# Kernel tuning notes

Measured on AMD Instinct MI355X. Metric: run time of the kernel, lower is better.

Reference implementation:

```python
import jax, jax.numpy as jnp
import numpy as np

B, T = 512, 2048
IN1, H1, H2 = 1, 64, 16


def _lstm_params(key, in_dim, hid):
    k = 1.0 / np.sqrt(hid)
    ks = jax.random.split(key, 4)
    u = lambda kk, shape: jax.random.uniform(kk, shape, jnp.float32, -k, k)
    return (u(ks[0], (4 * hid, in_dim)),  # w_ih, PyTorch gate order i,f,g,o
            u(ks[1], (4 * hid, hid)),     # w_hh
            u(ks[2], (4 * hid,)),         # b_ih
            u(ks[3], (4 * hid,)))         # b_hh


def setup_inputs() -> dict:
    key = jax.random.key(0)
    kx, k1, k2 = jax.random.split(key, 3)
    x = jax.random.normal(kx, (B, T, IN1), dtype=jnp.float32)
    w_ih1, w_hh1, b_ih1, b_hh1 = _lstm_params(k1, IN1, H1)
    w_ih2, w_hh2, b_ih2, b_hh2 = _lstm_params(k2, H1, H2)
    return {"x": x,
            "w_ih1": w_ih1, "w_hh1": w_hh1, "b_ih1": b_ih1, "b_hh1": b_hh1,
            "w_ih2": w_ih2, "w_hh2": w_hh2, "b_ih2": b_ih2, "b_hh2": b_hh2}


def _lstm(x, w_ih, w_hh, b_ih, b_hh):
    # x: [B, T, in]; returns all hidden states [B, T, H]
    hid = w_hh.shape[1]
    # precompute input contribution for every timestep: [T, B, 4H]
    xg = jnp.einsum('bti,gi->tbg', x, w_ih) + b_ih + b_hh
    h0 = jnp.zeros((x.shape[0], hid), x.dtype)
    c0 = jnp.zeros((x.shape[0], hid), x.dtype)

    def step(carry, xt):
        h, c = carry
        gates = xt + h @ w_hh.T                       # [B, 4H]
        i, f, g, o = jnp.split(gates, 4, axis=-1)     # PyTorch order
        i = jax.nn.sigmoid(i)
        f = jax.nn.sigmoid(f)
        g = jnp.tanh(g)
        o = jax.nn.sigmoid(o)
        c = f * c + i * g
        h = o * jnp.tanh(c)
        return (h, c), h

    _, hs = jax.lax.scan(step, (h0, c0), xg)          # hs: [T, B, H]
    return jnp.transpose(hs, (1, 0, 2))               # [B, T, H]


def reference(x, w_ih1, w_hh1, b_ih1, b_hh1, w_ih2, w_hh2, b_ih2, b_hh2):
    h1 = _lstm(x, w_ih1, w_hh1, b_ih1, b_hh1)   # [B, T, 64]
    h2 = _lstm(h1, w_ih2, w_hh2, b_ih2, b_hh2)  # [B, T, 16]
    return h2
```

## Files before the change

kernel.cpp:

```cpp
#include <hip/hip_runtime.h>

#define TSTEPS 2048
#define NBATCH 512
#define H1 64
#define H2 16

typedef _Float16 h2v __attribute__((ext_vector_type(2)));

__device__ __forceinline__ float fsig(float x) {
    return __builtin_amdgcn_rcpf(1.0f + __builtin_amdgcn_exp2f(-1.4426950408889634f * x));
}
__device__ __forceinline__ float ftanh(float x) {
    return 1.0f - 2.0f * __builtin_amdgcn_rcpf(1.0f + __builtin_amdgcn_exp2f(2.8853900817779268f * x));
}
__device__ __forceinline__ float act(float x, float k2) {
    return k2 * fsig(k2 * x) - (k2 - 1.0f);
}

#if __has_builtin(__builtin_amdgcn_fdot2)
__device__ __forceinline__ float dot2(int wp, int hp, float acc) {
    return __builtin_amdgcn_fdot2(__builtin_bit_cast(h2v, wp),
                                  __builtin_bit_cast(h2v, hp), acc, false);
}
#else
__device__ __forceinline__ float dot2(int wp, int hp, float acc) {
    h2v a = __builtin_bit_cast(h2v, wp), b = __builtin_bit_cast(h2v, hp);
    return acc + (float)a.x * (float)b.x + (float)a.y * (float)b.y;
}
#endif

__device__ __forceinline__ int packh2(float a, float b) {
    h2v v; v.x = (_Float16)a; v.y = (_Float16)b;
    return __builtin_bit_cast(int, v);
}
template<int CTRL>
__device__ __forceinline__ float dpp_bcast(float v) {
    int r = __builtin_amdgcn_mov_dpp(__float_as_int(v), CTRL, 0xF, 0xF, true);
    return __int_as_float(r);
}

__global__ void __launch_bounds__(64, 1)
__attribute__((amdgpu_waves_per_eu(1, 1)))
lstm2_fused(const float* __restrict__ x,
            const float* __restrict__ w_ih1,
            const float* __restrict__ w_hh1,
            const float* __restrict__ b_ih1,
            const float* __restrict__ b_hh1,
            const float* __restrict__ w_ih2,
            const float* __restrict__ w_hh2,
            const float* __restrict__ b_ih2,
            const float* __restrict__ b_hh2,
            float* __restrict__ out)
{
    const int lane = threadIdx.x;
    const int b    = blockIdx.x;

    __shared__ float    x_lds[TSTEPS];
    __shared__ _Float16 h1_lds[H1];
    __shared__ _Float16 h2_lds[H2];
    __shared__ float    ring[32][H2];

    {
        const float4* xs = (const float4*)(x + (size_t)b * TSTEPS);
        float4* xd = (float4*)x_lds;
        #pragma unroll
        for (int i = 0; i < 8; ++i) xd[lane + 64 * i] = xs[lane + 64 * i];
    }
    if (lane < 32) ((int*)h1_lds)[lane] = 0;
    if (lane < 8)  ((int*)h2_lds)[lane] = 0;

    int   w1[4][32];
    float wx1[4], bs1[4];
    #pragma unroll
    for (int g = 0; g < 4; ++g) {
        const int r = g * H1 + lane;
        const float* wr = w_hh1 + (size_t)r * H1;
        #pragma unroll
        for (int k = 0; k < 32; ++k) w1[g][k] = packh2(wr[2 * k], wr[2 * k + 1]);
        wx1[g] = w_ih1[r];
        bs1[g] = b_ih1[r] + b_hh1[r];
    }
    const int m  = lane >> 2;
    const int g2 = lane & 3;
    const int r2 = g2 * H2 + m;
    int w2[32], wh2[8];
    #pragma unroll
    for (int k = 0; k < 32; ++k)
        w2[k] = packh2(w_ih2[(size_t)r2 * H1 + 2 * k], w_ih2[(size_t)r2 * H1 + 2 * k + 1]);
    #pragma unroll
    for (int k = 0; k < 8; ++k)
        wh2[k] = packh2(w_hh2[(size_t)r2 * H2 + 2 * k], w_hh2[(size_t)r2 * H2 + 2 * k + 1]);
    const float bs2 = b_ih2[r2] + b_hh2[r2];
    const float k22 = (g2 == 2) ? 2.0f : 1.0f;

    float c1 = 0.0f;
    float c2 = 0.0f;
    float* outb = out + (size_t)b * TSTEPS * H2;

    for (int p = 0; p <= TSTEPS; ++p) {
        #pragma unroll
        for (int g = 0; g < 4; ++g)
            #pragma unroll
            for (int k = 0; k < 32; ++k) asm volatile("" : "+v"(w1[g][k]));
        #pragma unroll
        for (int k = 0; k < 32; ++k) asm volatile("" : "+v"(w2[k]));
        #pragma unroll
        for (int k = 0; k < 8; ++k)  asm volatile("" : "+v"(wh2[k]));

        const int tau_f = p - 1;
        if (tau_f >= 31 && (tau_f & 15) == 15) {
            const int tau0 = (tau_f & ~15) - 16;
            const int tt = tau0 + (lane >> 2), ch0 = (lane & 3) * 4;
            float4 v = *(const float4*)&ring[tt & 31][ch0];
            *(float4*)(outb + (size_t)tt * H2 + ch0) = v;
        }

        int hp[32];
        {
            const int4* hs = (const int4*)h1_lds;
            #pragma unroll
            for (int i = 0; i < 8; ++i) {
                int4 v = hs[i];
                hp[4*i+0] = v.x; hp[4*i+1] = v.y; hp[4*i+2] = v.z; hp[4*i+3] = v.w;
            }
        }

        if (p < TSTEPS) {
            const float xv = x_lds[p];
            float ai = bs1[0] + wx1[0] * xv;
            float af = bs1[1] + wx1[1] * xv;
            float ag = bs1[2] + wx1[2] * xv;
            float ao = bs1[3] + wx1[3] * xv;
            #pragma unroll
            for (int k = 0; k < 32; ++k) {
                ai = dot2(w1[0][k], hp[k], ai);
                af = dot2(w1[1][k], hp[k], af);
                ag = dot2(w1[2][k], hp[k], ag);
                ao = dot2(w1[3][k], hp[k], ao);
            }
            float gi = fsig(ai), gf = fsig(af), gg = ftanh(ag), go = fsig(ao);
            c1 = gf * c1 + gi * gg;
            float h1n = go * ftanh(c1);
            h1_lds[lane] = (_Float16)h1n;
        }

        if (p >= 1) {
            int hq[8];
            {
                const int4* hs = (const int4*)h2_lds;
                int4 u0 = hs[0], u1 = hs[1];
                hq[0]=u0.x; hq[1]=u0.y; hq[2]=u0.z; hq[3]=u0.w;
                hq[4]=u1.x; hq[5]=u1.y; hq[6]=u1.z; hq[7]=u1.w;
            }
            float a0 = bs2, a1 = 0.f, a2a = 0.f, a3 = 0.f;
            #pragma unroll
            for (int k = 0; k < 8; ++k) {
                a0  = dot2(w2[4*k+0], hp[4*k+0], a0);
                a1  = dot2(w2[4*k+1], hp[4*k+1], a1);
                a2a = dot2(w2[4*k+2], hp[4*k+2], a2a);
                a3  = dot2(w2[4*k+3], hp[4*k+3], a3);
            }
            #pragma unroll
            for (int k = 0; k < 2; ++k) {
                a0  = dot2(wh2[4*k+0], hq[4*k+0], a0);
                a1  = dot2(wh2[4*k+1], hq[4*k+1], a1);
                a2a = dot2(wh2[4*k+2], hq[4*k+2], a2a);
                a3  = dot2(wh2[4*k+3], hq[4*k+3], a3);
            }
            float av = act((a0 + a1) + (a2a + a3), k22);
            float gi = dpp_bcast<0x00>(av);
            float gf = dpp_bcast<0x55>(av);
            float gg = dpp_bcast<0xAA>(av);
            float go = dpp_bcast<0xFF>(av);
            c2 = gf * c2 + gi * gg;
            float h2n = go * ftanh(c2);
            if (g2 == 0) {
                h2_lds[m] = (_Float16)h2n;
                ring[(p - 1) & 31][m] = h2n;
            }
        }
    }

    {
        const int tt = 2032 + (lane >> 2), ch0 = (lane & 3) * 4;
        float4 v = *(const float4*)&ring[tt & 31][ch0];
        *(float4*)(outb + (size_t)tt * H2 + ch0) = v;
    }
}

extern "C" void kernel_launch(void* const* d_in, const int* in_sizes, int n_in,
                              void* d_out, int out_size, void* d_ws, size_t ws_size,
                              hipStream_t stream) {
    const float* x     = (const float*)d_in[0];
    const float* w_ih1 = (const float*)d_in[1];
    const float* w_hh1 = (const float*)d_in[2];
    const float* b_ih1 = (const float*)d_in[3];
    const float* b_hh1 = (const float*)d_in[4];
    const float* w_ih2 = (const float*)d_in[5];
    const float* w_hh2 = (const float*)d_in[6];
    const float* b_ih2 = (const float*)d_in[7];
    const float* b_hh2 = (const float*)d_in[8];
    float* out = (float*)d_out;

    lstm2_fused<<<NBATCH, 64, 0, stream>>>(x, w_ih1, w_hh1, b_ih1, b_hh1,
                                           w_ih2, w_hh2, b_ih2, b_hh2, out);
}
```

Measured before the change: 1.234 ms.

## Interleave layer-1 and layer-2 dot products with chunked LDS loads, pin weights in AGPRs

The layer-1 and layer-2 input-projection dot products now run in one loop over chunks of h1. Each chunk's LDS load is issued one iteration ahead so load latency hides behind the dot2 math, instead of loading all of h1 into registers up front. The layer-2 weights are pinned to accumulator registers (AGPRs) via inline asm constraints, and the occupancy attribute is replaced by a 256-VGPR cap to ease register pressure. The risk is extra AGPR-to-VGPR copies each step, and the layer-1 dot product now also runs on the final extra step (p == TSTEPS) with a wrapped x index.

```diff
diff --git a/kernel.cpp b/kernel.cpp
--- a/kernel.cpp
+++ b/kernel.cpp
@@ -40,7 +40,7 @@
 }
 
 __global__ void __launch_bounds__(64, 1)
-__attribute__((amdgpu_waves_per_eu(1, 1)))
+__attribute__((amdgpu_num_vgpr(256)))
 lstm2_fused(const float* __restrict__ x,
             const float* __restrict__ w_ih1,
             const float* __restrict__ w_hh1,
@@ -103,9 +103,9 @@
             #pragma unroll
             for (int k = 0; k < 32; ++k) asm volatile("" : "+v"(w1[g][k]));
         #pragma unroll
-        for (int k = 0; k < 32; ++k) asm volatile("" : "+v"(w2[k]));
-        #pragma unroll
-        for (int k = 0; k < 8; ++k)  asm volatile("" : "+v"(wh2[k]));
+        for (int k = 0; k < 32; ++k) asm volatile("" : "+a"(w2[k]));
+        #pragma unroll
+        for (int k = 0; k < 8; ++k)  asm volatile("" : "+a"(wh2[k]));
 
         const int tau_f = p - 1;
         if (tau_f >= 31 && (tau_f & 15) == 15) {
@@ -115,29 +115,47 @@
             *(float4*)(outb + (size_t)tt * H2 + ch0) = v;
         }
 
-        int hp[32];
+        const float xv = x_lds[p & (TSTEPS - 1)];
+        float ai = bs1[0] + wx1[0] * xv;
+        float af = bs1[1] + wx1[1] * xv;
+        float ag = bs1[2] + wx1[2] * xv;
+        float ao = bs1[3] + wx1[3] * xv;
+        float a0 = bs2, a1 = 0.f, a2a = 0.f, a3 = 0.f;
+
         {
-            const int4* hs = (const int4*)h1_lds;
+            const int4* hs4 = (const int4*)h1_lds;
+            int4 hA = hs4[0], hB = hs4[1];
             #pragma unroll
-            for (int i = 0; i < 8; ++i) {
-                int4 v = hs[i];
-                hp[4*i+0] = v.x; hp[4*i+1] = v.y; hp[4*i+2] = v.z; hp[4*i+3] = v.w;
+            for (int c = 0; c < 4; ++c) {
+                int4 nA, nB;
+                if (c < 3) { nA = hs4[2 * c + 2]; nB = hs4[2 * c + 3]; }
+                const int h0 = hA.x, h1p = hA.y, h2p = hA.z, h3p = hA.w;
+                const int h4p = hB.x, h5p = hB.y, h6p = hB.z, h7p = hB.w;
+                ai = dot2(w1[0][8*c+0], h0, ai);  af = dot2(w1[1][8*c+0], h0, af);
+                ag = dot2(w1[2][8*c+0], h0, ag);  ao = dot2(w1[3][8*c+0], h0, ao);
+                ai = dot2(w1[0][8*c+1], h1p, ai); af = dot2(w1[1][8*c+1], h1p, af);
+                ag = dot2(w1[2][8*c+1], h1p, ag); ao = dot2(w1[3][8*c+1], h1p, ao);
+                ai = dot2(w1[0][8*c+2], h2p, ai); af = dot2(w1[1][8*c+2], h2p, af);
+                ag = dot2(w1[2][8*c+2], h2p, ag); ao = dot2(w1[3][8*c+2], h2p, ao);
+                ai = dot2(w1[0][8*c+3], h3p, ai); af = dot2(w1[1][8*c+3], h3p, af);
+                ag = dot2(w1[2][8*c+3], h3p, ag); ao = dot2(w1[3][8*c+3], h3p, ao);
+                ai = dot2(w1[0][8*c+4], h4p, ai); af = dot2(w1[1][8*c+4], h4p, af);
+                ag = dot2(w1[2][8*c+4], h4p, ag); ao = dot2(w1[3][8*c+4], h4p, ao);
+                ai = dot2(w1[0][8*c+5], h5p, ai); af = dot2(w1[1][8*c+5], h5p, af);
+                ag = dot2(w1[2][8*c+5], h5p, ag); ao = dot2(w1[3][8*c+5], h5p, ao);
+                ai = dot2(w1[0][8*c+6], h6p, ai); af = dot2(w1[1][8*c+6], h6p, af);
+                ag = dot2(w1[2][8*c+6], h6p, ag); ao = dot2(w1[3][8*c+6], h6p, ao);
+                ai = dot2(w1[0][8*c+7], h7p, ai); af = dot2(w1[1][8*c+7], h7p, af);
+                ag = dot2(w1[2][8*c+7], h7p, ag); ao = dot2(w1[3][8*c+7], h7p, ao);
+                a0  = dot2(w2[8*c+0], h0,  a0);   a0  = dot2(w2[8*c+4], h4p, a0);
+                a1  = dot2(w2[8*c+1], h1p, a1);   a1  = dot2(w2[8*c+5], h5p, a1);
+                a2a = dot2(w2[8*c+2], h2p, a2a);  a2a = dot2(w2[8*c+6], h6p, a2a);
+                a3  = dot2(w2[8*c+3], h3p, a3);   a3  = dot2(w2[8*c+7], h7p, a3);
+                if (c < 3) { hA = nA; hB = nB; }
             }
         }
 
         if (p < TSTEPS) {
-            const float xv = x_lds[p];
-            float ai = bs1[0] + wx1[0] * xv;
-            float af = bs1[1] + wx1[1] * xv;
-            float ag = bs1[2] + wx1[2] * xv;
-            float ao = bs1[3] + wx1[3] * xv;
-            #pragma unroll
-            for (int k = 0; k < 32; ++k) {
-                ai = dot2(w1[0][k], hp[k], ai);
-                af = dot2(w1[1][k], hp[k], af);
-                ag = dot2(w1[2][k], hp[k], ag);
-                ao = dot2(w1[3][k], hp[k], ao);
-            }
             float gi = fsig(ai), gf = fsig(af), gg = ftanh(ag), go = fsig(ao);
             c1 = gf * c1 + gi * gg;
             float h1n = go * ftanh(c1);
@@ -151,14 +169,6 @@
                 int4 u0 = hs[0], u1 = hs[1];
                 hq[0]=u0.x; hq[1]=u0.y; hq[2]=u0.z; hq[3]=u0.w;
                 hq[4]=u1.x; hq[5]=u1.y; hq[6]=u1.z; hq[7]=u1.w;
-            }
-            float a0 = bs2, a1 = 0.f, a2a = 0.f, a3 = 0.f;
-            #pragma unroll
-            for (int k = 0; k < 8; ++k) {
-                a0  = dot2(w2[4*k+0], hp[4*k+0], a0);
-                a1  = dot2(w2[4*k+1], hp[4*k+1], a1);
-                a2a = dot2(w2[4*k+2], hp[4*k+2], a2a);
-                a3  = dot2(w2[4*k+3], hp[4*k+3], a3);
             }
             #pragma unroll
             for (int k = 0; k < 2; ++k) {
```

Result: slower. 1.359 ms (+10.1%).

## Split each batch's recurrent dot products across two waves with LDS exchange

Applied to the files above, without the earlier changes.

Each block now runs two waves. Each wave holds half of the K dimension of the layer-1 and layer-2 weights and computes partial gate sums, then the waves swap partials through double-buffered LDS with a block barrier every timestep. Both waves then finish the activations redundantly and write their own copy of the hidden state. This halves the serial dot-product chain per timestep and the register pressure per lane. The cost is a __syncthreads plus LDS round trip on the critical path of every step, and 512 blocks of 128 threads instead of 64.

```diff
diff --git a/kernel.cpp b/kernel.cpp
--- a/kernel.cpp
+++ b/kernel.cpp
@@ -39,7 +39,7 @@
     return __int_as_float(r);
 }
 
-__global__ void __launch_bounds__(64, 1)
+__global__ void __launch_bounds__(128, 1)
 __attribute__((amdgpu_waves_per_eu(1, 1)))
 lstm2_fused(const float* __restrict__ x,
             const float* __restrict__ w_ih1,
@@ -52,44 +52,51 @@
             const float* __restrict__ b_hh2,
             float* __restrict__ out)
 {
-    const int lane = threadIdx.x;
+    const int tid  = threadIdx.x;
+    const int w    = tid >> 6;
+    const int lane = tid & 63;
     const int b    = blockIdx.x;
 
-    __shared__ float    x_lds[TSTEPS];
-    __shared__ _Float16 h1_lds[H1];
-    __shared__ _Float16 h2_lds[H2];
-    __shared__ float    ring[32][H2];
-
+    __shared__ __align__(16) float    x_lds[TSTEPS];
+    __shared__ __align__(16) _Float16 h1s[2][H1];
+    __shared__ __align__(16) _Float16 h2s[2][H2];
+    __shared__ __align__(16) float    xch[2][2][64][4];
+    __shared__ __align__(16) float    xch2[2][2][64];
+    __shared__ __align__(16) float    ring[32][H2];
+
+    if (tid < 64) ((int*)h1s)[tid] = 0;
+    else if (tid < 80) ((int*)h2s)[tid - 64] = 0;
     {
         const float4* xs = (const float4*)(x + (size_t)b * TSTEPS);
         float4* xd = (float4*)x_lds;
         #pragma unroll
-        for (int i = 0; i < 8; ++i) xd[lane + 64 * i] = xs[lane + 64 * i];
-    }
-    if (lane < 32) ((int*)h1_lds)[lane] = 0;
-    if (lane < 8)  ((int*)h2_lds)[lane] = 0;
-
-    int   w1[4][32];
+        for (int i = 0; i < 4; ++i) xd[tid + 128 * i] = xs[tid + 128 * i];
+    }
+    __syncthreads();
+
+    int   w1[4][16];
     float wx1[4], bs1[4];
     #pragma unroll
     for (int g = 0; g < 4; ++g) {
         const int r = g * H1 + lane;
-        const float* wr = w_hh1 + (size_t)r * H1;
+        const float* wr = w_hh1 + (size_t)r * H1 + 32 * w;
         #pragma unroll
-        for (int k = 0; k < 32; ++k) w1[g][k] = packh2(wr[2 * k], wr[2 * k + 1]);
+        for (int t = 0; t < 16; ++t) w1[g][t] = packh2(wr[2 * t], wr[2 * t + 1]);
         wx1[g] = w_ih1[r];
         bs1[g] = b_ih1[r] + b_hh1[r];
     }
     const int m  = lane >> 2;
     const int g2 = lane & 3;
     const int r2 = g2 * H2 + m;
-    int w2[32], wh2[8];
+    int w2[16], wh2[4];
     #pragma unroll
-    for (int k = 0; k < 32; ++k)
-        w2[k] = packh2(w_ih2[(size_t)r2 * H1 + 2 * k], w_ih2[(size_t)r2 * H1 + 2 * k + 1]);
+    for (int t = 0; t < 16; ++t)
+        w2[t] = packh2(w_ih2[(size_t)r2 * H1 + 32 * w + 2 * t],
+                       w_ih2[(size_t)r2 * H1 + 32 * w + 2 * t + 1]);
     #pragma unroll
-    for (int k = 0; k < 8; ++k)
-        wh2[k] = packh2(w_hh2[(size_t)r2 * H2 + 2 * k], w_hh2[(size_t)r2 * H2 + 2 * k + 1]);
+    for (int t = 0; t < 4; ++t)
+        wh2[t] = packh2(w_hh2[(size_t)r2 * H2 + 8 * w + 2 * t],
+                        w_hh2[(size_t)r2 * H2 + 8 * w + 2 * t + 1]);
     const float bs2 = b_ih2[r2] + b_hh2[r2];
     const float k22 = (g2 == 2) ? 2.0f : 1.0f;
 
@@ -97,77 +104,66 @@
     float c2 = 0.0f;
     float* outb = out + (size_t)b * TSTEPS * H2;
 
+    const int4* hs = ((const int4*)h1s[w]) + 4 * w;
+
+#define DOTP(T, HV)  do {                                   \
+        ai = dot2(w1[0][T], HV, ai);                        \
+        af = dot2(w1[1][T], HV, af);                        \
+        ag = dot2(w1[2][T], HV, ag);                        \
+        ao = dot2(w1[3][T], HV, ao);                        \
+        if ((T & 3) == 0) a0 = dot2(w2[T], HV, a0);         \
+        if ((T & 3) == 1) a1 = dot2(w2[T], HV, a1);         \
+        if ((T & 3) == 2) a2 = dot2(w2[T], HV, a2);         \
+        if ((T & 3) == 3) a3 = dot2(w2[T], HV, a3);         \
+    } while (0)
+
     for (int p = 0; p <= TSTEPS; ++p) {
-        #pragma unroll
-        for (int g = 0; g < 4; ++g)
-            #pragma unroll
-            for (int k = 0; k < 32; ++k) asm volatile("" : "+v"(w1[g][k]));
-        #pragma unroll
-        for (int k = 0; k < 32; ++k) asm volatile("" : "+v"(w2[k]));
-        #pragma unroll
-        for (int k = 0; k < 8; ++k)  asm volatile("" : "+v"(wh2[k]));
-
         const int tau_f = p - 1;
         if (tau_f >= 31 && (tau_f & 15) == 15) {
             const int tau0 = (tau_f & ~15) - 16;
-            const int tt = tau0 + (lane >> 2), ch0 = (lane & 3) * 4;
-            float4 v = *(const float4*)&ring[tt & 31][ch0];
-            *(float4*)(outb + (size_t)tt * H2 + ch0) = v;
+            const int tt = tau0 + (tid >> 3), ch0 = (tid & 7) * 2;
+            float2 v = *(const float2*)&ring[tt & 31][ch0];
+            *(float2*)(outb + (size_t)tt * H2 + ch0) = v;
         }
 
-        int hp[32];
-        {
-            const int4* hs = (const int4*)h1_lds;
-            #pragma unroll
-            for (int i = 0; i < 8; ++i) {
-                int4 v = hs[i];
-                hp[4*i+0] = v.x; hp[4*i+1] = v.y; hp[4*i+2] = v.z; hp[4*i+3] = v.w;
-            }
-        }
+        int4 hA = hs[0], hB = hs[1], hC = hs[2], hD = hs[3];
+        int4 hq = ((const int4*)h2s[w])[w];
+
+        float ai = 0.f, af = 0.f, ag = 0.f, ao = 0.f;
+        float a0 = 0.f, a1 = 0.f, a2 = 0.f, a3 = 0.f;
+        DOTP(0, hA.x);  DOTP(1, hA.y);  DOTP(2, hA.z);  DOTP(3, hA.w);
+        DOTP(4, hB.x);  DOTP(5, hB.y);  DOTP(6, hB.z);  DOTP(7, hB.w);
+        DOTP(8, hC.x);  DOTP(9, hC.y);  DOTP(10, hC.z); DOTP(11, hC.w);
+        DOTP(12, hD.x); DOTP(13, hD.y); DOTP(14, hD.z); DOTP(15, hD.w);
+        a0 = dot2(wh2[0], hq.x, a0);
+        a1 = dot2(wh2[1], hq.y, a1);
+        a2 = dot2(wh2[2], hq.z, a2);
+        a3 = dot2(wh2[3], hq.w, a3);
+        const float my2 = (a0 + a1) + (a2 + a3);
+
+        const int pb = p & 1;
+        float4 mine = {ai, af, ag, ao};
+        *(float4*)&xch[pb][w][lane][0] = mine;
+        xch2[pb][w][lane] = my2;
+        __syncthreads();
+        float4 othr = *(const float4*)&xch[pb][w ^ 1][lane][0];
+        float  o2   = xch2[pb][w ^ 1][lane];
 
         if (p < TSTEPS) {
             const float xv = x_lds[p];
-            float ai = bs1[0] + wx1[0] * xv;
-            float af = bs1[1] + wx1[1] * xv;
-            float ag = bs1[2] + wx1[2] * xv;
-            float ao = bs1[3] + wx1[3] * xv;
-            #pragma unroll
-            for (int k = 0; k < 32; ++k) {
-                ai = dot2(w1[0][k], hp[k], ai);
-                af = dot2(w1[1][k], hp[k], af);
-                ag = dot2(w1[2][k], hp[k], ag);
-                ao = dot2(w1[3][k], hp[k], ao);
-            }
-            float gi = fsig(ai), gf = fsig(af), gg = ftanh(ag), go = fsig(ao);
+            float pi = ai + othr.x + bs1[0] + wx1[0] * xv;
+            float pf = af + othr.y + bs1[1] + wx1[1] * xv;
+            float pg = ag + othr.z + bs1[2] + wx1[2] * xv;
+            float po = ao + othr.w + bs1[3] + wx1[3] * xv;
+            float gi = fsig(pi), gf = fsig(pf), gg = ftanh(pg), go = fsig(po);
             c1 = gf * c1 + gi * gg;
             float h1n = go * ftanh(c1);
-            h1_lds[lane] = (_Float16)h1n;
+            h1s[w][lane] = (_Float16)h1n;
         }
 
         if (p >= 1) {
-            int hq[8];
-            {
-                const int4* hs = (const int4*)h2_lds;
-                int4 u0 = hs[0], u1 = hs[1];
-                hq[0]=u0.x; hq[1]=u0.y; hq[2]=u0.z; hq[3]=u0.w;
-                hq[4]=u1.x; hq[5]=u1.y; hq[6]=u1.z; hq[7]=u1.w;
-            }
-            float a0 = bs2, a1 = 0.f, a2a = 0.f, a3 = 0.f;
-            #pragma unroll
-            for (int k = 0; k < 8; ++k) {
-                a0  = dot2(w2[4*k+0], hp[4*k+0], a0);
-                a1  = dot2(w2[4*k+1], hp[4*k+1], a1);
-                a2a = dot2(w2[4*k+2], hp[4*k+2], a2a);
-                a3  = dot2(w2[4*k+3], hp[4*k+3], a3);
-            }
-            #pragma unroll
-            for (int k = 0; k < 2; ++k) {
-                a0  = dot2(wh2[4*k+0], hq[4*k+0], a0);
-                a1  = dot2(wh2[4*k+1], hq[4*k+1], a1);
-                a2a = dot2(wh2[4*k+2], hq[4*k+2], a2a);
-                a3  = dot2(wh2[4*k+3], hq[4*k+3], a3);
-            }
-            float av = act((a0 + a1) + (a2a + a3), k22);
+            float pre2 = my2 + o2 + bs2;
+            float av = act(pre2, k22);
             float gi = dpp_bcast<0x00>(av);
             float gf = dpp_bcast<0x55>(av);
             float gg = dpp_bcast<0xAA>(av);
@@ -175,16 +171,19 @@
             c2 = gf * c2 + gi * gg;
             float h2n = go * ftanh(c2);
             if (g2 == 0) {
-                h2_lds[m] = (_Float16)h2n;
-                ring[(p - 1) & 31][m] = h2n;
+                h2s[w][m] = (_Float16)h2n;
+                if (w == 0) ring[(p - 1) & 31][m] = h2n;
             }
         }
     }
+#undef DOTP
+
+    __syncthreads();
 
     {
-        const int tt = 2032 + (lane >> 2), ch0 = (lane & 3) * 4;
-        float4 v = *(const float4*)&ring[tt & 31][ch0];
-        *(float4*)(outb + (size_t)tt * H2 + ch0) = v;
+        const int tt = 2032 + (tid >> 3), ch0 = (tid & 7) * 2;
+        float2 v = *(const float2*)&ring[tt & 31][ch0];
+        *(float2*)(outb + (size_t)tt * H2 + ch0) = v;
     }
 }
 
@@ -202,6 +201,6 @@
     const float* b_hh2 = (const float*)d_in[8];
     float* out = (float*)d_out;
 
-    lstm2_fused<<<NBATCH, 64, 0, stream>>>(x, w_ih1, w_hh1, b_ih1, b_hh1,
-                                           w_ih2, w_hh2, b_ih2, b_hh2, out);
-}
+    lstm2_fused<<<NBATCH, 128, 0, stream>>>(x, w_ih1, w_hh1, b_ih1, b_hh1,
+                                            w_ih2, w_hh2, b_ih2, b_hh2, out);
+}
```

Result: slower. 1.588 ms (+28.7%).

## Move g/o gate and layer-2 weights from registers into LDS

Applied to the files above, without the earlier changes.

Keeps only the input and forget gate recurrent weights in VGPRs and stages the cell and output gate weights plus layer-2 weights as packed half2 in shared memory, loading them each timestep interleaved with the dot products. It also merges the layer-2 input projection into the same loop over h1 chunks. The aim is lower register pressure and better scheduling, at the cost of extra LDS reads per step in a latency-bound recurrence.

```diff
diff --git a/kernel.cpp b/kernel.cpp
--- a/kernel.cpp
+++ b/kernel.cpp
@@ -55,6 +55,7 @@
     const int lane = threadIdx.x;
     const int b    = blockIdx.x;
 
+    __shared__ int4     wlds[26][64];
     __shared__ float    x_lds[TSTEPS];
     __shared__ _Float16 h1_lds[H1];
     __shared__ _Float16 h2_lds[H2];
@@ -69,27 +70,48 @@
     if (lane < 32) ((int*)h1_lds)[lane] = 0;
     if (lane < 8)  ((int*)h2_lds)[lane] = 0;
 
-    int   w1[4][32];
-    float wx1[4], bs1[4];
-    #pragma unroll
-    for (int g = 0; g < 4; ++g) {
-        const int r = g * H1 + lane;
-        const float* wr = w_hh1 + (size_t)r * H1;
+    int w1i[32], w1f[32];
+    {
+        const float* wri = w_hh1 + (size_t)lane * H1;
+        const float* wrf = w_hh1 + (size_t)(H1 + lane) * H1;
         #pragma unroll
-        for (int k = 0; k < 32; ++k) w1[g][k] = packh2(wr[2 * k], wr[2 * k + 1]);
-        wx1[g] = w_ih1[r];
-        bs1[g] = b_ih1[r] + b_hh1[r];
+        for (int k = 0; k < 32; ++k) {
+            w1i[k] = packh2(wri[2 * k], wri[2 * k + 1]);
+            w1f[k] = packh2(wrf[2 * k], wrf[2 * k + 1]);
+        }
     }
     const int m  = lane >> 2;
     const int g2 = lane & 3;
     const int r2 = g2 * H2 + m;
-    int w2[32], wh2[8];
-    #pragma unroll
-    for (int k = 0; k < 32; ++k)
-        w2[k] = packh2(w_ih2[(size_t)r2 * H1 + 2 * k], w_ih2[(size_t)r2 * H1 + 2 * k + 1]);
-    #pragma unroll
-    for (int k = 0; k < 8; ++k)
-        wh2[k] = packh2(w_hh2[(size_t)r2 * H2 + 2 * k], w_hh2[(size_t)r2 * H2 + 2 * k + 1]);
+    {
+        const float* wrg = w_hh1 + (size_t)(2 * H1 + lane) * H1;
+        const float* wro = w_hh1 + (size_t)(3 * H1 + lane) * H1;
+        const float* wr2 = w_ih2 + (size_t)r2 * H1;
+        #pragma unroll
+        for (int tq = 0; tq < 8; ++tq) {
+            wlds[tq][lane] = make_int4(
+                packh2(wrg[8*tq+0], wrg[8*tq+1]), packh2(wrg[8*tq+2], wrg[8*tq+3]),
+                packh2(wrg[8*tq+4], wrg[8*tq+5]), packh2(wrg[8*tq+6], wrg[8*tq+7]));
+            wlds[8 + tq][lane] = make_int4(
+                packh2(wro[8*tq+0], wro[8*tq+1]), packh2(wro[8*tq+2], wro[8*tq+3]),
+                packh2(wro[8*tq+4], wro[8*tq+5]), packh2(wro[8*tq+6], wro[8*tq+7]));
+            wlds[16 + tq][lane] = make_int4(
+                packh2(wr2[8*tq+0], wr2[8*tq+1]), packh2(wr2[8*tq+2], wr2[8*tq+3]),
+                packh2(wr2[8*tq+4], wr2[8*tq+5]), packh2(wr2[8*tq+6], wr2[8*tq+7]));
+        }
+        const float* wrh = w_hh2 + (size_t)r2 * H2;
+        wlds[24][lane] = make_int4(packh2(wrh[0], wrh[1]),  packh2(wrh[2], wrh[3]),
+                                   packh2(wrh[4], wrh[5]),  packh2(wrh[6], wrh[7]));
+        wlds[25][lane] = make_int4(packh2(wrh[8], wrh[9]),  packh2(wrh[10], wrh[11]),
+                                   packh2(wrh[12], wrh[13]), packh2(wrh[14], wrh[15]));
+    }
+
+    const float wxi = w_ih1[lane],        wxf = w_ih1[H1 + lane];
+    const float wxg = w_ih1[2*H1 + lane], wxo = w_ih1[3*H1 + lane];
+    const float bsi = b_ih1[lane] + b_hh1[lane];
+    const float bsf = b_ih1[H1+lane] + b_hh1[H1+lane];
+    const float bsg = b_ih1[2*H1+lane] + b_hh1[2*H1+lane];
+    const float bso = b_ih1[3*H1+lane] + b_hh1[3*H1+lane];
     const float bs2 = b_ih2[r2] + b_hh2[r2];
     const float k22 = (g2 == 2) ? 2.0f : 1.0f;
 
@@ -97,16 +119,9 @@
     float c2 = 0.0f;
     float* outb = out + (size_t)b * TSTEPS * H2;
 
+    const int4* wl = &wlds[0][0];
+
     for (int p = 0; p <= TSTEPS; ++p) {
-        #pragma unroll
-        for (int g = 0; g < 4; ++g)
-            #pragma unroll
-            for (int k = 0; k < 32; ++k) asm volatile("" : "+v"(w1[g][k]));
-        #pragma unroll
-        for (int k = 0; k < 32; ++k) asm volatile("" : "+v"(w2[k]));
-        #pragma unroll
-        for (int k = 0; k < 8; ++k)  asm volatile("" : "+v"(wh2[k]));
-
         const int tau_f = p - 1;
         if (tau_f >= 31 && (tau_f & 15) == 15) {
             const int tau0 = (tau_f & ~15) - 16;
@@ -115,29 +130,55 @@
             *(float4*)(outb + (size_t)tt * H2 + ch0) = v;
         }
 
-        int hp[32];
+        const float xv = x_lds[p & (TSTEPS - 1)];
+        float ai = bsi + wxi * xv;
+        float af = bsf + wxf * xv;
+        float ag = bsg + wxg * xv;
+        float ao = bso + wxo * xv;
+        float a0 = bs2, a1 = 0.f, a2a = 0.f, a3 = 0.f;
+        int4 vh0, vh1;
+
         {
-            const int4* hs = (const int4*)h1_lds;
+            const int4* hs4 = (const int4*)h1_lds;
             #pragma unroll
-            for (int i = 0; i < 8; ++i) {
-                int4 v = hs[i];
-                hp[4*i+0] = v.x; hp[4*i+1] = v.y; hp[4*i+2] = v.z; hp[4*i+3] = v.w;
+            for (int c = 0; c < 4; ++c) {
+                int4 hA = hs4[2*c], hB = hs4[2*c + 1];
+                int4 cg  = wl[(2*c)      * 64 + lane];
+                int4 cg2 = wl[(2*c + 1)  * 64 + lane];
+                int4 co  = wl[(8 + 2*c)  * 64 + lane];
+                int4 co2 = wl[(9 + 2*c)  * 64 + lane];
+                int4 cu  = wl[(16 + 2*c) * 64 + lane];
+                int4 cu2 = wl[(17 + 2*c) * 64 + lane];
+                if (c == 2) { vh0 = wl[24 * 64 + lane]; vh1 = wl[25 * 64 + lane]; }
+
+                ai = dot2(w1i[8*c+0], hA.x, ai); ai = dot2(w1i[8*c+1], hA.y, ai);
+                ai = dot2(w1i[8*c+2], hA.z, ai); ai = dot2(w1i[8*c+3], hA.w, ai);
+                ai = dot2(w1i[8*c+4], hB.x, ai); ai = dot2(w1i[8*c+5], hB.y, ai);
+                ai = dot2(w1i[8*c+6], hB.z, ai); ai = dot2(w1i[8*c+7], hB.w, ai);
+
+                af = dot2(w1f[8*c+0], hA.x, af); af = dot2(w1f[8*c+1], hA.y, af);
+                af = dot2(w1f[8*c+2], hA.z, af); af = dot2(w1f[8*c+3], hA.w, af);
+                af = dot2(w1f[8*c+4], hB.x, af); af = dot2(w1f[8*c+5], hB.y, af);
+                af = dot2(w1f[8*c+6], hB.z, af); af = dot2(w1f[8*c+7], hB.w, af);
+
+                ag = dot2(cg.x,  hA.x, ag); ag = dot2(cg.y,  hA.y, ag);
+                ag = dot2(cg.z,  hA.z, ag); ag = dot2(cg.w,  hA.w, ag);
+                ag = dot2(cg2.x, hB.x, ag); ag = dot2(cg2.y, hB.y, ag);
+                ag = dot2(cg2.z, hB.z, ag); ag = dot2(cg2.w, hB.w, ag);
+
+                ao = dot2(co.x,  hA.x, ao); ao = dot2(co.y,  hA.y, ao);
+                ao = dot2(co.z,  hA.z, ao); ao = dot2(co.w,  hA.w, ao);
+                ao = dot2(co2.x, hB.x, ao); ao = dot2(co2.y, hB.y, ao);
+                ao = dot2(co2.z, hB.z, ao); ao = dot2(co2.w, hB.w, ao);
+
+                a0  = dot2(cu.x,  hA.x, a0);  a1  = dot2(cu.y,  hA.y, a1);
+                a2a = dot2(cu.z,  hA.z, a2a); a3  = dot2(cu.w,  hA.w, a3);
+                a0  = dot2(cu2.x, hB.x, a0);  a1  = dot2(cu2.y, hB.y, a1);
+                a2a = dot2(cu2.z, hB.z, a2a); a3  = dot2(cu2.w, hB.w, a3);
             }
         }
 
         if (p < TSTEPS) {
-            const float xv = x_lds[p];
-            float ai = bs1[0] + wx1[0] * xv;
-            float af = bs1[1] + wx1[1] * xv;
-            float ag = bs1[2] + wx1[2] * xv;
-            float ao = bs1[3] + wx1[3] * xv;
-            #pragma unroll
-            for (int k = 0; k < 32; ++k) {
-                ai = dot2(w1[0][k], hp[k], ai);
-                af = dot2(w1[1][k], hp[k], af);
-                ag = dot2(w1[2][k], hp[k], ag);
-                ao = dot2(w1[3][k], hp[k], ao);
-            }
             float gi = fsig(ai), gf = fsig(af), gg = ftanh(ag), go = fsig(ao);
             c1 = gf * c1 + gi * gg;
             float h1n = go * ftanh(c1);
@@ -145,28 +186,12 @@
         }
 
         if (p >= 1) {
-            int hq[8];
-            {
-                const int4* hs = (const int4*)h2_lds;
-                int4 u0 = hs[0], u1 = hs[1];
-                hq[0]=u0.x; hq[1]=u0.y; hq[2]=u0.z; hq[3]=u0.w;
-                hq[4]=u1.x; hq[5]=u1.y; hq[6]=u1.z; hq[7]=u1.w;
-            }
-            float a0 = bs2, a1 = 0.f, a2a = 0.f, a3 = 0.f;
-            #pragma unroll
-            for (int k = 0; k < 8; ++k) {
-                a0  = dot2(w2[4*k+0], hp[4*k+0], a0);
-                a1  = dot2(w2[4*k+1], hp[4*k+1], a1);
-                a2a = dot2(w2[4*k+2], hp[4*k+2], a2a);
-                a3  = dot2(w2[4*k+3], hp[4*k+3], a3);
-            }
-            #pragma unroll
-            for (int k = 0; k < 2; ++k) {
-                a0  = dot2(wh2[4*k+0], hq[4*k+0], a0);
-                a1  = dot2(wh2[4*k+1], hq[4*k+1], a1);
-                a2a = dot2(wh2[4*k+2], hq[4*k+2], a2a);
-                a3  = dot2(wh2[4*k+3], hq[4*k+3], a3);
-            }
+            const int4* hs = (const int4*)h2_lds;
+            int4 u0 = hs[0], u1 = hs[1];
+            a0  = dot2(vh0.x, u0.x, a0);  a1  = dot2(vh0.y, u0.y, a1);
+            a2a = dot2(vh0.z, u0.z, a2a); a3  = dot2(vh0.w, u0.w, a3);
+            a0  = dot2(vh1.x, u1.x, a0);  a1  = dot2(vh1.y, u1.y, a1);
+            a2a = dot2(vh1.z, u1.z, a2a); a3  = dot2(vh1.w, u1.w, a3);
             float av = act((a0 + a1) + (a2a + a3), k22);
             float gi = dpp_bcast<0x00>(av);
             float gf = dpp_bcast<0x55>(av);
```

Result: faster. 1.170 ms, median of 2 (-5.2%).
